# Optimization experiments

Hardware: AMD Instinct MI355X
Metric: run time of the kernel (lower is better)

## Reference

```python
import jax, jax.numpy as jnp
import numpy as np

BETA = 0.9       # membrane decay factor
THRESHOLD = 1.0  # firing threshold
ALPHA = 2.0      # atan surrogate slope (snntorch default)

@jax.custom_vjp
def spike(x):
    # Heaviside spike on (mem - threshold)
    return (x > 0).astype(x.dtype)

def _spike_fwd(x):
    return (x > 0).astype(x.dtype), x

def _spike_bwd(x, g):
    # atan surrogate: d spk / d x = (alpha/2) / (1 + (pi/2 * alpha * x)^2)
    return (g * (ALPHA / 2.0) / (1.0 + (jnp.pi / 2.0 * ALPHA * x) ** 2),)

spike.defvjp(_spike_fwd, _spike_bwd)


def snn_forward(x, params):
    """x: (T, B, F_in); params: list of (W[out,in], b[out]).
    Returns (spike_record (T,B,out), final membrane (B,out)).
    Dropout is identity (eval mode). LIF: mem=beta*mem+cur; spk=H(mem-thr); mem-=spk*thr."""
    B = x.shape[1]
    mems0 = tuple(jnp.zeros((B, W.shape[0]), x.dtype) for W, _ in params)

    def step(mems, xt):
        h = xt
        new_mems = []
        for (W, b), m in zip(params, mems):
            cur = h @ W.T + b                 # (B, out)
            m = BETA * m + cur                # leaky integrate
            s = spike(m - THRESHOLD)          # fire
            m = m - s * THRESHOLD             # subtract reset
            new_mems.append(m)
            h = s                             # spikes feed next layer
        return tuple(new_mems), (h, new_mems[-1])

    _, (spks, mem_rec) = jax.lax.scan(step, mems0, x)
    return spks, mem_rec[-1]


def _linear_init(key, out_f, in_f):
    k1, k2 = jax.random.split(key)
    bound = 1.0 / np.sqrt(in_f)
    W = jax.random.uniform(k1, (out_f, in_f), jnp.float32, -bound, bound)
    b = jax.random.uniform(k2, (out_f,), jnp.float32, -bound, bound)
    return W, b


def setup_inputs() -> dict:
    key = jax.random.key(0)
    ks = jax.random.split(key, 4)
    T, B = 25, 256
    sizes = [1024, 2048, 2048, 1024]
    x = jax.random.normal(ks[0], (T, B, sizes[0]), jnp.float32)
    w0, b0 = _linear_init(ks[1], sizes[1], sizes[0])
    w1, b1 = _linear_init(ks[2], sizes[2], sizes[1])
    w2, b2 = _linear_init(ks[3], sizes[3], sizes[2])
    return {"x": x, "w0": w0, "b0": b0, "w1": w1, "b1": b1, "w2": w2, "b2": b2}


def reference(x, w0, b0, w1, b1, w2, b2):
    return snn_forward(x, [(w0, b0), (w1, b1), (w2, b2)])
```

## Files before the change

kernel.cpp:

```cpp
#include <hip/hip_runtime.h>
#include <hip/hip_bf16.h>

typedef __bf16 bf16;
typedef __bf16 bf16x4 __attribute__((ext_vector_type(4)));
typedef __bf16 bf16x8 __attribute__((ext_vector_type(8)));
typedef float  f32x4  __attribute__((ext_vector_type(4)));

#define DEVFN static __device__ __forceinline__

static constexpr int T_STEPS = 25;
static constexpr int BATCH   = 256;
static constexpr int MROWS   = T_STEPS * BATCH;

DEVFN void llds16(const void* g, void* l) {
    __builtin_amdgcn_global_load_lds(
        (const __attribute__((address_space(1))) void*)g,
        (__attribute__((address_space(3))) void*)l, 16, 0, 0);
}

DEVFN void split3_chunk(const float* src, bf16* p0, bf16* p1, bf16* p2, int i) {
    float4 v = *(const float4*)(src + i);
    float vv[4] = {v.x, v.y, v.z, v.w};
    bf16x4 a, b, c;
#pragma unroll
    for (int k = 0; k < 4; ++k) {
        bf16 h0 = (bf16)vv[k];
        float r1 = vv[k] - (float)h0;
        bf16 h1 = (bf16)r1;
        float r2 = r1 - (float)h1;
        a[k] = h0; b[k] = h1; c[k] = (bf16)r2;
    }
    *(bf16x4*)(p0 + i) = a;
    *(bf16x4*)(p1 + i) = b;
    *(bf16x4*)(p2 + i) = c;
}

DEVFN void split2_chunk(const float* src, bf16* p0, bf16* p1, int i) {
    float4 v = *(const float4*)(src + i);
    float vv[4] = {v.x, v.y, v.z, v.w};
    bf16x4 a, b;
#pragma unroll
    for (int k = 0; k < 4; ++k) {
        bf16 h0 = (bf16)vv[k];
        a[k] = h0; b[k] = (bf16)(vv[k] - (float)h0);
    }
    *(bf16x4*)(p0 + i) = a;
    *(bf16x4*)(p1 + i) = b;
}

static constexpr int SB_W0 = 2048;
static constexpr int SB_W1 = 4096;
static constexpr int SB_W2 = 2048;
static constexpr int SB_X  = 6400;

__global__ void split_all(const float* __restrict__ w0, bf16* w0p0, bf16* w0p1, bf16* w0p2,
                          const float* __restrict__ w1, bf16* w1p0, bf16* w1p1, bf16* w1p2,
                          const float* __restrict__ w2, bf16* w2p0, bf16* w2p1,
                          const float* __restrict__ x,  bf16* xp0,  bf16* xp1,  bf16* xp2) {
    int b = blockIdx.x;
    if (b < SB_W0) {
        split3_chunk(w0, w0p0, w0p1, w0p2, b * 1024 + threadIdx.x * 4);
    } else if (b < SB_W0 + SB_W1) {
        split3_chunk(w1, w1p0, w1p1, w1p2, (b - SB_W0) * 1024 + threadIdx.x * 4);
    } else if (b < SB_W0 + SB_W1 + SB_W2) {
        split2_chunk(w2, w2p0, w2p1, (b - SB_W0 - SB_W1) * 1024 + threadIdx.x * 4);
    } else {
        split3_chunk(x, xp0, xp1, xp2, (b - SB_W0 - SB_W1 - SB_W2) * 1024 + threadIdx.x * 4);
    }
}


struct TileCtx { int t, lane, wm, wn, bm, bn, fr, fkS, cr, cc; };

DEVFN TileCtx make_ctx512() {
    TileCtx x;
    x.t = threadIdx.x; x.lane = x.t & 63;
    int wv = x.t >> 6;
    x.wm = (wv >> 1) * 64;
    x.wn = (wv & 1) * 64;
    x.bm = blockIdx.x * 256; x.bn = blockIdx.y * 128;
    x.fr  = x.lane & 15;
    x.fkS = (((x.lane >> 4) ^ ((x.lane >> 1) & 3))) * 16;
    x.cr = (x.lane >> 4) * 4; x.cc = x.lane & 15;
    return x;
}

template <int ROWS>
DEVFN void stage(const bf16* g, bf16* s, int base_row, int K, int k0, int t) {
#pragma unroll
    for (int r = 0; r < ROWS / 128; ++r) {
        int c   = t + r * 512;
        int row = c >> 2;
        int kc  = (((c & 3) ^ ((c >> 3) & 3))) * 8;
        llds16(g + (size_t)(base_row + row) * K + k0 + kc,
               (bf16*)((char*)s + (c >> 6) * 1024));
    }
}

DEVFN void frag4(bf16x8* f, const bf16* s, int wrow, int fr, int fkS) {
#pragma unroll
    for (int i = 0; i < 4; ++i)
        f[i] = *(const bf16x8*)((const char*)s + (wrow + i * 16 + fr) * 64 + fkS);
}

DEVFN void mfma16(f32x4 (&acc)[4][4], const bf16x8* a, const bf16x8* b) {
    __builtin_amdgcn_s_setprio(1);
#pragma unroll
    for (int i = 0; i < 4; ++i)
#pragma unroll
        for (int j = 0; j < 4; ++j)
            acc[i][j] = __builtin_amdgcn_mfma_f32_16x16x32_bf16(a[i], b[j], acc[i][j], 0, 0, 0);
    __builtin_amdgcn_s_setprio(0);
}

DEVFN void epilogue(const f32x4 (&accM)[4][4], const f32x4 (&accS)[4][4],
                    const float* bias, float* C, int N, const TileCtx& x) {
#pragma unroll
    for (int j = 0; j < 4; ++j) {
        int col   = x.bn + x.wn + j * 16 + x.cc;
        double bv = (double)bias[col];
#pragma unroll
        for (int i = 0; i < 4; ++i) {
            int row0 = x.bm + x.wm + i * 16 + x.cr;
#pragma unroll
            for (int r = 0; r < 4; ++r) {
                double v = (double)accM[i][j][r] + (double)accS[i][j][r] + bv;
                C[(size_t)(row0 + r) * N + col] = (float)v;
            }
        }
    }
}

template <int MODE>
__global__ __launch_bounds__(512, 2)
void gemm_ph(const bf16* __restrict__ A0, const bf16* __restrict__ A1,
             const bf16* __restrict__ A2, const bf16* __restrict__ B0,
             const bf16* __restrict__ B1, const bf16* __restrict__ B2,
             const float* __restrict__ bias, float* __restrict__ C,
             int M, int N, int K) {
    constexpr int NA  = (MODE == 0) ? 3 : 1;
    constexpr int NB  = (MODE == 2) ? 2 : 3;
    constexpr int APL = 256 * 32;
    constexpr int BPL = 128 * 32;
    constexpr int BUF = NA * APL + NB * BPL;
    __shared__ __align__(1024) bf16 lds[2 * BUF];

    TileCtx x = make_ctx512();
    f32x4 accM[4][4] = {}, accS[4][4] = {};

    auto pA = [&](int p, int i) { return lds + p * BUF + i * APL; };
    auto pB = [&](int p, int i) { return lds + p * BUF + NA * APL + i * BPL; };

    auto stage_all = [&](int p, int k0) {
        stage<256>(A0, pA(p, 0), x.bm, K, k0, x.t);
        if constexpr (MODE == 0) {
            stage<256>(A1, pA(p, 1), x.bm, K, k0, x.t);
            stage<256>(A2, pA(p, 2), x.bm, K, k0, x.t);
        }
        stage<128>(B0, pB(p, 0), x.bn, K, k0, x.t);
        stage<128>(B1, pB(p, 1), x.bn, K, k0, x.t);
        if constexpr (NB == 3) stage<128>(B2, pB(p, 2), x.bn, K, k0, x.t);
    };

    stage_all(0, 0);
    __syncthreads();

    const int NT = K / 32;
    int p = 0;
    for (int tt = 0; tt < NT; ++tt, p ^= 1) {
        if (tt + 1 < NT) stage_all(p ^ 1, (tt + 1) * 32);

        bf16x8 a[4], b0f[4], b1f[4], b2f[4];
        if constexpr (MODE == 0) {
            frag4(a,   pA(p, 0), x.wm, x.fr, x.fkS);
            frag4(b0f, pB(p, 0), x.wn, x.fr, x.fkS);
            mfma16(accM, a, b0f);
            frag4(b1f, pB(p, 1), x.wn, x.fr, x.fkS);
            mfma16(accS, a, b1f);
            frag4(b2f, pB(p, 2), x.wn, x.fr, x.fkS);
            mfma16(accS, a, b2f);
            frag4(a, pA(p, 1), x.wm, x.fr, x.fkS);
            mfma16(accS, a, b0f);
            mfma16(accS, a, b1f);
            frag4(a, pA(p, 2), x.wm, x.fr, x.fkS);
            mfma16(accS, a, b0f);
        } else if constexpr (MODE == 1) {
            frag4(a,   pA(p, 0), x.wm, x.fr, x.fkS);
            frag4(b0f, pB(p, 0), x.wn, x.fr, x.fkS);
            mfma16(accM, a, b0f);
            frag4(b1f, pB(p, 1), x.wn, x.fr, x.fkS);
            mfma16(accS, a, b1f);
            frag4(b2f, pB(p, 2), x.wn, x.fr, x.fkS);
            mfma16(accS, a, b2f);
        } else {
            frag4(a,   pA(p, 0), x.wm, x.fr, x.fkS);
            frag4(b0f, pB(p, 0), x.wn, x.fr, x.fkS);
            mfma16(accM, a, b0f);
            frag4(b1f, pB(p, 1), x.wn, x.fr, x.fkS);
            mfma16(accS, a, b1f);
        }
        __syncthreads();
    }
    epilogue(accM, accS, bias, C, N, x);
}

template <int F>
__global__ void lif_hidden(const float* __restrict__ cur, bf16* __restrict__ spk) {
    const int tid = blockIdx.x * 256 + threadIdx.x;
    double m = 0.0;
    size_t off = tid;
#pragma unroll
    for (int t = 0; t < T_STEPS; ++t) {
        m = 0.9 * m + (double)cur[off];
        bool s = (m - 1.0) > 0.0;
        spk[off] = (bf16)(s ? 1.0f : 0.0f);
        if (s) m -= 1.0;
        off += (size_t)BATCH * F;
    }
}

__global__ void lif_out(const float* __restrict__ cur, float* __restrict__ out) {
    const int tid = blockIdx.x * 256 + threadIdx.x;
    double m = 0.0;
    size_t off = tid;
#pragma unroll
    for (int t = 0; t < T_STEPS; ++t) {
        m = 0.9 * m + (double)cur[off];
        bool s = (m - 1.0) > 0.0;
        out[off] = s ? 1.0f : 0.0f;
        if (s) m -= 1.0;
        off += (size_t)BATCH * 1024;
    }
    out[(size_t)T_STEPS * BATCH * 1024 + tid] = (float)m;
}

extern "C" void kernel_launch(void* const* d_in, const int* in_sizes, int n_in,
                              void* d_out, int out_size, void* d_ws, size_t ws_size,
                              hipStream_t stream) {
    const float* xin = (const float*)d_in[0];
    const float* w0  = (const float*)d_in[1];
    const float* b0  = (const float*)d_in[2];
    const float* w1  = (const float*)d_in[3];
    const float* b1  = (const float*)d_in[4];
    const float* w2  = (const float*)d_in[5];
    const float* b2  = (const float*)d_in[6];
    float* out = (float*)d_out;

    constexpr size_t NW0 = 2048 * 1024;
    constexpr size_t NW1 = 2048 * 2048;
    constexpr size_t NW2 = 1024 * 2048;
    constexpr size_t NX  = (size_t)MROWS * 1024;
    constexpr size_t NH  = (size_t)MROWS * 2048;

    char* ws = (char*)d_ws;
    size_t off = 0;
    auto carve = [&](size_t bytes) { char* p = ws + off; off += bytes; return p; };

    bf16* w1p0 = (bf16*)carve(NW1 * 2);
    bf16* w1p1 = (bf16*)carve(NW1 * 2);
    bf16* w1p2 = (bf16*)carve(NW1 * 2);
    bf16* w2p0 = (bf16*)carve(NW2 * 2);
    bf16* w2p1 = (bf16*)carve(NW2 * 2);
    char* pool = carve(2 * NH * 2);
    bf16* w0p0 = (bf16*)pool;
    bf16* w0p1 = w0p0 + NW0;
    bf16* w0p2 = w0p1 + NW0;
    bf16* xp0  = w0p2 + NW0;
    bf16* xp1  = xp0 + NX;
    bf16* xp2  = xp1 + NX;
    bf16* s0   = (bf16*)pool;
    bf16* s1   = s0 + NH;
    float* cur = (float*)carve(NH * 4);
    if (ws_size < off) return;

    split_all<<<SB_W0 + SB_W1 + SB_W2 + SB_X, 256, 0, stream>>>(
        w0, w0p0, w0p1, w0p2, w1, w1p0, w1p1, w1p2,
        w2, w2p0, w2p1, xin, xp0, xp1, xp2);

    gemm_ph<0><<<dim3(25, 16), 512, 0, stream>>>(xp0, xp1, xp2, w0p0, w0p1, w0p2,
                                                 b0, cur, MROWS, 2048, 1024);
    lif_hidden<2048><<<(BATCH * 2048) / 256, 256, 0, stream>>>(cur, s0);

    gemm_ph<1><<<dim3(25, 16), 512, 0, stream>>>(s0, nullptr, nullptr, w1p0, w1p1, w1p2,
                                                 b1, cur, MROWS, 2048, 2048);
    lif_hidden<2048><<<(BATCH * 2048) / 256, 256, 0, stream>>>(cur, s1);

    gemm_ph<2><<<dim3(25, 8), 512, 0, stream>>>(s1, nullptr, nullptr, w2p0, w2p1, nullptr,
                                                b2, cur, MROWS, 1024, 2048);
    lif_out<<<(BATCH * 1024) / 256, 256, 0, stream>>>(cur, out);
}
```

Before: 512.1 us.

## Use int8 MFMA with fixed-point weight splits for spike-input GEMMs

```diff
diff --git a/kernel.cpp b/kernel.cpp
--- a/kernel.cpp
+++ b/kernel.cpp
@@ -5,6 +5,9 @@
 typedef __bf16 bf16x4 __attribute__((ext_vector_type(4)));
 typedef __bf16 bf16x8 __attribute__((ext_vector_type(8)));
 typedef float  f32x4  __attribute__((ext_vector_type(4)));
+typedef signed char i8;
+typedef signed char i8x4 __attribute__((ext_vector_type(4)));
+typedef int    i32x4 __attribute__((ext_vector_type(4)));
 
 #define DEVFN static __device__ __forceinline__
 
@@ -35,17 +38,33 @@
     *(bf16x4*)(p2 + i) = c;
 }
 
-DEVFN void split2_chunk(const float* src, bf16* p0, bf16* p1, int i) {
+DEVFN void spliti8_3(const float* src, i8* p0, i8* p1, i8* p2, int i) {
     float4 v = *(const float4*)(src + i);
     float vv[4] = {v.x, v.y, v.z, v.w};
-    bf16x4 a, b;
+    i8x4 a, b, c;
 #pragma unroll
     for (int k = 0; k < 4; ++k) {
-        bf16 h0 = (bf16)vv[k];
-        a[k] = h0; b[k] = (bf16)(vv[k] - (float)h0);
-    }
-    *(bf16x4*)(p0 + i) = a;
-    *(bf16x4*)(p1 + i) = b;
+        float t  = vv[k] * 4096.0f;
+        float q0 = rintf(t);  float r = t - q0;
+        float q1 = rintf(r * 128.0f); r = r * 128.0f - q1;
+        float q2 = rintf(r * 128.0f);
+        a[k] = (i8)(int)q0; b[k] = (i8)(int)q1; c[k] = (i8)(int)q2;
+    }
+    *(i8x4*)(p0 + i) = a; *(i8x4*)(p1 + i) = b; *(i8x4*)(p2 + i) = c;
+}
+
+DEVFN void spliti8_2(const float* src, i8* p0, i8* p1, int i) {
+    float4 v = *(const float4*)(src + i);
+    float vv[4] = {v.x, v.y, v.z, v.w};
+    i8x4 a, b;
+#pragma unroll
+    for (int k = 0; k < 4; ++k) {
+        float t  = vv[k] * 4096.0f;
+        float q0 = rintf(t);  float r = t - q0;
+        float q1 = rintf(r * 128.0f);
+        a[k] = (i8)(int)q0; b[k] = (i8)(int)q1;
+    }
+    *(i8x4*)(p0 + i) = a; *(i8x4*)(p1 + i) = b;
 }
 
 static constexpr int SB_W0 = 2048;
@@ -54,53 +73,19 @@
 static constexpr int SB_X  = 6400;
 
 __global__ void split_all(const float* __restrict__ w0, bf16* w0p0, bf16* w0p1, bf16* w0p2,
-                          const float* __restrict__ w1, bf16* w1p0, bf16* w1p1, bf16* w1p2,
-                          const float* __restrict__ w2, bf16* w2p0, bf16* w2p1,
+                          const float* __restrict__ w1, i8* w1q0, i8* w1q1, i8* w1q2,
+                          const float* __restrict__ w2, i8* w2q0, i8* w2q1,
                           const float* __restrict__ x,  bf16* xp0,  bf16* xp1,  bf16* xp2) {
     int b = blockIdx.x;
     if (b < SB_W0) {
         split3_chunk(w0, w0p0, w0p1, w0p2, b * 1024 + threadIdx.x * 4);
     } else if (b < SB_W0 + SB_W1) {
-        split3_chunk(w1, w1p0, w1p1, w1p2, (b - SB_W0) * 1024 + threadIdx.x * 4);
+        spliti8_3(w1, w1q0, w1q1, w1q2, (b - SB_W0) * 1024 + threadIdx.x * 4);
     } else if (b < SB_W0 + SB_W1 + SB_W2) {
-        split2_chunk(w2, w2p0, w2p1, (b - SB_W0 - SB_W1) * 1024 + threadIdx.x * 4);
+        spliti8_2(w2, w2q0, w2q1, (b - SB_W0 - SB_W1) * 1024 + threadIdx.x * 4);
     } else {
         split3_chunk(x, xp0, xp1, xp2, (b - SB_W0 - SB_W1 - SB_W2) * 1024 + threadIdx.x * 4);
     }
-}
-
-
-struct TileCtx { int t, lane, wm, wn, bm, bn, fr, fkS, cr, cc; };
-
-DEVFN TileCtx make_ctx512() {
-    TileCtx x;
-    x.t = threadIdx.x; x.lane = x.t & 63;
-    int wv = x.t >> 6;
-    x.wm = (wv >> 1) * 64;
-    x.wn = (wv & 1) * 64;
-    x.bm = blockIdx.x * 256; x.bn = blockIdx.y * 128;
-    x.fr  = x.lane & 15;
-    x.fkS = (((x.lane >> 4) ^ ((x.lane >> 1) & 3))) * 16;
-    x.cr = (x.lane >> 4) * 4; x.cc = x.lane & 15;
-    return x;
-}
-
-template <int ROWS>
-DEVFN void stage(const bf16* g, bf16* s, int base_row, int K, int k0, int t) {
-#pragma unroll
-    for (int r = 0; r < ROWS / 128; ++r) {
-        int c   = t + r * 512;
-        int row = c >> 2;
-        int kc  = (((c & 3) ^ ((c >> 3) & 3))) * 8;
-        llds16(g + (size_t)(base_row + row) * K + k0 + kc,
-               (bf16*)((char*)s + (c >> 6) * 1024));
-    }
-}
-
-DEVFN void frag4(bf16x8* f, const bf16* s, int wrow, int fr, int fkS) {
-#pragma unroll
-    for (int i = 0; i < 4; ++i)
-        f[i] = *(const bf16x8*)((const char*)s + (wrow + i * 16 + fr) * 64 + fkS);
 }
 
 DEVFN void mfma16(f32x4 (&acc)[4][4], const bf16x8* a, const bf16x8* b) {
@@ -113,99 +98,233 @@
     __builtin_amdgcn_s_setprio(0);
 }
 
-DEVFN void epilogue(const f32x4 (&accM)[4][4], const f32x4 (&accS)[4][4],
-                    const float* bias, float* C, int N, const TileCtx& x) {
-#pragma unroll
-    for (int j = 0; j < 4; ++j) {
-        int col   = x.bn + x.wn + j * 16 + x.cc;
-        double bv = (double)bias[col];
-#pragma unroll
-        for (int i = 0; i < 4; ++i) {
-            int row0 = x.bm + x.wm + i * 16 + x.cr;
-#pragma unroll
-            for (int r = 0; r < 4; ++r) {
-                double v = (double)accM[i][j][r] + (double)accS[i][j][r] + bv;
-                C[(size_t)(row0 + r) * N + col] = (float)v;
-            }
-        }
-    }
-}
-
-template <int MODE>
+DEVFN void frag4b(bf16x8* f, const bf16* s, int wrow, int fr, int fkS) {
+#pragma unroll
+    for (int i = 0; i < 4; ++i)
+        f[i] = *(const bf16x8*)((const char*)s + (wrow + i * 16 + fr) * 64 + fkS);
+}
+
 __global__ __launch_bounds__(512, 2)
-void gemm_ph(const bf16* __restrict__ A0, const bf16* __restrict__ A1,
+void gemm_l0(const bf16* __restrict__ A0, const bf16* __restrict__ A1,
              const bf16* __restrict__ A2, const bf16* __restrict__ B0,
              const bf16* __restrict__ B1, const bf16* __restrict__ B2,
              const float* __restrict__ bias, float* __restrict__ C,
              int M, int N, int K) {
-    constexpr int NA  = (MODE == 0) ? 3 : 1;
-    constexpr int NB  = (MODE == 2) ? 2 : 3;
     constexpr int APL = 256 * 32;
     constexpr int BPL = 128 * 32;
-    constexpr int BUF = NA * APL + NB * BPL;
+    constexpr int BUF = 3 * APL + 3 * BPL;
     __shared__ __align__(1024) bf16 lds[2 * BUF];
 
-    TileCtx x = make_ctx512();
+    const int t = threadIdx.x, lane = t & 63, wv = t >> 6;
+    const int wm = (wv >> 1) * 64, wn = (wv & 1) * 64;
+    const int bm = blockIdx.x * 256, bn = blockIdx.y * 128;
+    const int sk = (wv >> 2) & 1;
+    const int fr = lane & 15, g = lane >> 4;
+    const int fkS = (g ^ ((lane >> 1) & 3)) * 16;
+    const int cr = g * 4, cc = fr;
+
     f32x4 accM[4][4] = {}, accS[4][4] = {};
 
     auto pA = [&](int p, int i) { return lds + p * BUF + i * APL; };
-    auto pB = [&](int p, int i) { return lds + p * BUF + NA * APL + i * BPL; };
-
-    auto stage_all = [&](int p, int k0) {
-        stage<256>(A0, pA(p, 0), x.bm, K, k0, x.t);
-        if constexpr (MODE == 0) {
-            stage<256>(A1, pA(p, 1), x.bm, K, k0, x.t);
-            stage<256>(A2, pA(p, 2), x.bm, K, k0, x.t);
-        }
-        stage<128>(B0, pB(p, 0), x.bn, K, k0, x.t);
-        stage<128>(B1, pB(p, 1), x.bn, K, k0, x.t);
-        if constexpr (NB == 3) stage<128>(B2, pB(p, 2), x.bn, K, k0, x.t);
+    auto pB = [&](int p, int i) { return lds + p * BUF + 3 * APL + i * BPL; };
+
+    int offA[2], offB[1];
+#pragma unroll
+    for (int r = 0; r < 2; ++r) {
+        int c = t + r * 512, row = c >> 2, slot = c & 3;
+        offA[r] = (bm + row) * K + (slot ^ ((row >> 1) & 3)) * 8;
+    }
+    {
+        int c = t, row = c >> 2, slot = c & 3;
+        offB[0] = (bn + row) * K + (slot ^ ((row >> 1) & 3)) * 8;
+    }
+    auto stA = [&](const bf16* gp, bf16* s, int k0) {
+#pragma unroll
+        for (int r = 0; r < 2; ++r)
+            llds16(gp + offA[r] + k0, (char*)s + ((t + r * 512) >> 6) * 1024);
     };
-
-    stage_all(0, 0);
+    auto stB = [&](const bf16* gp, bf16* s, int k0) {
+        llds16(gp + offB[0] + k0, (char*)s + (t >> 6) * 1024);
+    };
+
+    stA(A0, pA(0, 0), 0); stA(A1, pA(0, 1), 0); stA(A2, pA(0, 2), 0);
+    stB(B0, pB(0, 0), 0); stB(B1, pB(0, 1), 0); stB(B2, pB(0, 2), 0);
     __syncthreads();
 
     const int NT = K / 32;
     int p = 0;
     for (int tt = 0; tt < NT; ++tt, p ^= 1) {
-        if (tt + 1 < NT) stage_all(p ^ 1, (tt + 1) * 32);
-
+        const int q = p ^ 1, kn = (tt + 1) * 32;
+        const bool pf = (tt + 1 < NT);
         bf16x8 a[4], b0f[4], b1f[4], b2f[4];
-        if constexpr (MODE == 0) {
-            frag4(a,   pA(p, 0), x.wm, x.fr, x.fkS);
-            frag4(b0f, pB(p, 0), x.wn, x.fr, x.fkS);
+        if (sk == 0) {
+            frag4b(a,   pA(p, 0), wm, fr, fkS);
+            frag4b(b0f, pB(p, 0), wn, fr, fkS);
+            if (pf) stA(A0, pA(q, 0), kn);
             mfma16(accM, a, b0f);
-            frag4(b1f, pB(p, 1), x.wn, x.fr, x.fkS);
+            if (pf) { stA(A1, pA(q, 1), kn); stA(A2, pA(q, 2), kn); }
+            frag4b(b1f, pB(p, 1), wn, fr, fkS);
             mfma16(accS, a, b1f);
-            frag4(b2f, pB(p, 2), x.wn, x.fr, x.fkS);
+            if (pf) { stB(B0, pB(q, 0), kn); stB(B1, pB(q, 1), kn); stB(B2, pB(q, 2), kn); }
+            frag4b(b2f, pB(p, 2), wn, fr, fkS);
             mfma16(accS, a, b2f);
-            frag4(a, pA(p, 1), x.wm, x.fr, x.fkS);
+            frag4b(a, pA(p, 1), wm, fr, fkS);
             mfma16(accS, a, b0f);
             mfma16(accS, a, b1f);
-            frag4(a, pA(p, 2), x.wm, x.fr, x.fkS);
+            frag4b(a, pA(p, 2), wm, fr, fkS);
             mfma16(accS, a, b0f);
-        } else if constexpr (MODE == 1) {
-            frag4(a,   pA(p, 0), x.wm, x.fr, x.fkS);
-            frag4(b0f, pB(p, 0), x.wn, x.fr, x.fkS);
+        } else {
+            frag4b(a,   pA(p, 1), wm, fr, fkS);
+            frag4b(b0f, pB(p, 0), wn, fr, fkS);
+            if (pf) stA(A0, pA(q, 0), kn);
+            mfma16(accS, a, b0f);
+            if (pf) { stA(A1, pA(q, 1), kn); stA(A2, pA(q, 2), kn); }
+            frag4b(b1f, pB(p, 1), wn, fr, fkS);
+            mfma16(accS, a, b1f);
+            if (pf) { stB(B0, pB(q, 0), kn); stB(B1, pB(q, 1), kn); stB(B2, pB(q, 2), kn); }
+            frag4b(a, pA(p, 2), wm, fr, fkS);
+            mfma16(accS, a, b0f);
+            frag4b(a, pA(p, 0), wm, fr, fkS);
             mfma16(accM, a, b0f);
-            frag4(b1f, pB(p, 1), x.wn, x.fr, x.fkS);
+            frag4b(b2f, pB(p, 2), wn, fr, fkS);
             mfma16(accS, a, b1f);
-            frag4(b2f, pB(p, 2), x.wn, x.fr, x.fkS);
             mfma16(accS, a, b2f);
-        } else {
-            frag4(a,   pA(p, 0), x.wm, x.fr, x.fkS);
-            frag4(b0f, pB(p, 0), x.wn, x.fr, x.fkS);
-            mfma16(accM, a, b0f);
-            frag4(b1f, pB(p, 1), x.wn, x.fr, x.fkS);
-            mfma16(accS, a, b1f);
         }
         __syncthreads();
     }
-    epilogue(accM, accS, bias, C, N, x);
+
+#pragma unroll
+    for (int j = 0; j < 4; ++j) {
+        int col = bn + wn + j * 16 + cc;
+        double bvs = (double)bias[col];
+#pragma unroll
+        for (int i = 0; i < 4; ++i) {
+            int row0 = bm + wm + i * 16 + cr;
+#pragma unroll
+            for (int r = 0; r < 4; ++r) {
+                double v = (double)accM[i][j][r] + (double)accS[i][j][r] + bvs;
+                C[(size_t)(row0 + r) * N + col] = (float)v;
+            }
+        }
+    }
+}
+
+template <int MODE>
+__global__ __launch_bounds__(512, 2)
+void gemm_i8(const i8* __restrict__ A, const i8* __restrict__ B0,
+             const i8* __restrict__ B1, const i8* __restrict__ B2,
+             const float* __restrict__ bias, float* __restrict__ C,
+             int M, int N, int K) {
+    constexpr int NP  = (MODE == 1) ? 3 : 2;
+    constexpr int BN  = (MODE == 1) ? 64 : 128;
+    constexpr int WNF = (MODE == 1) ? 2 : 4;
+    constexpr int BK  = 128;
+    constexpr int APL = 256 * BK;
+    constexpr int BPL = BN * BK;
+    constexpr int BUF = APL + NP * BPL;
+    constexpr int AIT = 4;
+    constexpr int BIT = (BN * 8) / 512;
+    __shared__ __align__(1024) i8 lds[2 * BUF];
+
+    const int t = threadIdx.x, lane = t & 63, wv = t >> 6;
+    const int wm = (wv >> 1) * 64, wn = (wv & 1) * (WNF * 16);
+    const int bm = blockIdx.x * 256, bn = blockIdx.y * BN;
+    const int fr = lane & 15, g = lane >> 4;
+    const int fkA = (g ^ (lane & 7)) * 16;
+    const int fkB = ((4 + g) ^ (lane & 7)) * 16;
+    const int cr = g * 4, cc = fr;
+
+    i32x4 acc[NP][4][WNF] = {};
+
+    int offA[AIT], offB[BIT];
+#pragma unroll
+    for (int r = 0; r < AIT; ++r) {
+        int c = t + r * 512, row = c >> 3, slot = c & 7;
+        offA[r] = (bm + row) * K + (slot ^ (row & 7)) * 16;
+    }
+#pragma unroll
+    for (int r = 0; r < BIT; ++r) {
+        int c = t + r * 512, row = c >> 3, slot = c & 7;
+        offB[r] = (bn + row) * K + (slot ^ (row & 7)) * 16;
+    }
+    auto stA = [&](const i8* gp, i8* s, int k0) {
+#pragma unroll
+        for (int r = 0; r < AIT; ++r)
+            llds16(gp + offA[r] + k0, s + ((t + r * 512) >> 6) * 1024);
+    };
+    auto stB = [&](const i8* gp, i8* s, int k0) {
+#pragma unroll
+        for (int r = 0; r < BIT; ++r)
+            llds16(gp + offB[r] + k0, s + ((t + r * 512) >> 6) * 1024);
+    };
+    auto pAl = [&](int p) { return lds + p * BUF; };
+    auto pBl = [&](int p, int pl) { return lds + p * BUF + APL + pl * BPL; };
+
+    stA(A, pAl(0), 0);
+    stB(B0, pBl(0, 0), 0);
+    stB(B1, pBl(0, 1), 0);
+    if constexpr (NP == 3) stB(B2, pBl(0, 2), 0);
+    __syncthreads();
+
+    const int NT = K / BK;
+    int p = 0;
+    for (int tt = 0; tt < NT; ++tt, p ^= 1) {
+        const int q = p ^ 1, kn = (tt + 1) * BK;
+        const bool pf = (tt + 1 < NT);
+        const i8* sA = pAl(p);
+        i32x4 av[4], bvf[NP][WNF];
+#pragma unroll
+        for (int kh = 0; kh < 2; ++kh) {
+            const int fk = kh ? fkB : fkA;
+#pragma unroll
+            for (int i = 0; i < 4; ++i)
+                av[i] = *(const i32x4*)(sA + (wm + i * 16 + fr) * 128 + fk);
+            if (kh == 0 && pf) stA(A, pAl(q), kn);
+#pragma unroll
+            for (int pl = 0; pl < NP; ++pl) {
+                const i8* sB = pBl(p, pl);
+#pragma unroll
+                for (int j = 0; j < WNF; ++j)
+                    bvf[pl][j] = *(const i32x4*)(sB + (wn + j * 16 + fr) * 128 + fk);
+            }
+            if (kh == 0 && pf) {
+                stB(B0, pBl(q, 0), kn);
+                stB(B1, pBl(q, 1), kn);
+                if constexpr (NP == 3) stB(B2, pBl(q, 2), kn);
+            }
+            __builtin_amdgcn_s_setprio(1);
+#pragma unroll
+            for (int pl = 0; pl < NP; ++pl)
+#pragma unroll
+                for (int i = 0; i < 4; ++i)
+#pragma unroll
+                    for (int j = 0; j < WNF; ++j)
+                        acc[pl][i][j] = __builtin_amdgcn_mfma_i32_16x16x64_i8(
+                            av[i], bvf[pl][j], acc[pl][i][j], 0, 0, 0);
+            __builtin_amdgcn_s_setprio(0);
+        }
+        __syncthreads();
+    }
+
+#pragma unroll
+    for (int j = 0; j < WNF; ++j) {
+        int col = bn + wn + j * 16 + cc;
+        double bvs = (double)bias[col];
+#pragma unroll
+        for (int i = 0; i < 4; ++i) {
+            int row0 = bm + wm + i * 16 + cr;
+#pragma unroll
+            for (int r = 0; r < 4; ++r) {
+                double v = (double)acc[0][i][j][r] + (double)acc[1][i][j][r] * (1.0 / 128.0);
+                if constexpr (NP == 3) v += (double)acc[2][i][j][r] * (1.0 / 16384.0);
+                C[(size_t)(row0 + r) * N + col] = (float)(v * (1.0 / 4096.0) + bvs);
+            }
+        }
+    }
 }
 
 template <int F>
-__global__ void lif_hidden(const float* __restrict__ cur, bf16* __restrict__ spk) {
+__global__ void lif_hidden(const float* __restrict__ cur, i8* __restrict__ spk) {
     const int tid = blockIdx.x * 256 + threadIdx.x;
     double m = 0.0;
     size_t off = tid;
@@ -213,7 +332,7 @@
     for (int t = 0; t < T_STEPS; ++t) {
         m = 0.9 * m + (double)cur[off];
         bool s = (m - 1.0) > 0.0;
-        spk[off] = (bf16)(s ? 1.0f : 0.0f);
+        spk[off] = s ? (i8)1 : (i8)0;
         if (s) m -= 1.0;
         off += (size_t)BATCH * F;
     }
@@ -256,11 +375,11 @@
     size_t off = 0;
     auto carve = [&](size_t bytes) { char* p = ws + off; off += bytes; return p; };
 
-    bf16* w1p0 = (bf16*)carve(NW1 * 2);
-    bf16* w1p1 = (bf16*)carve(NW1 * 2);
-    bf16* w1p2 = (bf16*)carve(NW1 * 2);
-    bf16* w2p0 = (bf16*)carve(NW2 * 2);
-    bf16* w2p1 = (bf16*)carve(NW2 * 2);
+    i8* w1q0 = (i8*)carve(NW1);
+    i8* w1q1 = (i8*)carve(NW1);
+    i8* w1q2 = (i8*)carve(NW1);
+    i8* w2q0 = (i8*)carve(NW2);
+    i8* w2q1 = (i8*)carve(NW2);
     char* pool = carve(2 * NH * 2);
     bf16* w0p0 = (bf16*)pool;
     bf16* w0p1 = w0p0 + NW0;
@@ -268,24 +387,24 @@
     bf16* xp0  = w0p2 + NW0;
     bf16* xp1  = xp0 + NX;
     bf16* xp2  = xp1 + NX;
-    bf16* s0   = (bf16*)pool;
-    bf16* s1   = s0 + NH;
+    i8* s0 = (i8*)pool;
+    i8* s1 = s0 + NH;
     float* cur = (float*)carve(NH * 4);
     if (ws_size < off) return;
 
     split_all<<<SB_W0 + SB_W1 + SB_W2 + SB_X, 256, 0, stream>>>(
-        w0, w0p0, w0p1, w0p2, w1, w1p0, w1p1, w1p2,
-        w2, w2p0, w2p1, xin, xp0, xp1, xp2);
-
-    gemm_ph<0><<<dim3(25, 16), 512, 0, stream>>>(xp0, xp1, xp2, w0p0, w0p1, w0p2,
-                                                 b0, cur, MROWS, 2048, 1024);
+        w0, w0p0, w0p1, w0p2, w1, w1q0, w1q1, w1q2,
+        w2, w2q0, w2q1, xin, xp0, xp1, xp2);
+
+    gemm_l0<<<dim3(25, 16), 512, 0, stream>>>(xp0, xp1, xp2, w0p0, w0p1, w0p2,
+                                              b0, cur, MROWS, 2048, 1024);
     lif_hidden<2048><<<(BATCH * 2048) / 256, 256, 0, stream>>>(cur, s0);
 
-    gemm_ph<1><<<dim3(25, 16), 512, 0, stream>>>(s0, nullptr, nullptr, w1p0, w1p1, w1p2,
+    gemm_i8<1><<<dim3(25, 32), 512, 0, stream>>>(s0, w1q0, w1q1, w1q2,
                                                  b1, cur, MROWS, 2048, 2048);
     lif_hidden<2048><<<(BATCH * 2048) / 256, 256, 0, stream>>>(cur, s1);
 
-    gemm_ph<2><<<dim3(25, 8), 512, 0, stream>>>(s1, nullptr, nullptr, w2p0, w2p1, nullptr,
+    gemm_i8<2><<<dim3(25, 8), 512, 0, stream>>>(s1, w2q0, w2q1, nullptr,
                                                 b2, cur, MROWS, 1024, 2048);
     lif_out<<<(BATCH * 1024) / 256, 256, 0, stream>>>(cur, out);
 }
```

After: 412.4 us. -19.5%, faster.
